# Optimization experiments

Measured on AMD Instinct MI355X. Metric: run time of the kernel, lower is better.

Reference implementation:

```python
import jax, jax.numpy as jnp
import numpy as np

FFT_N = 320.0  # one-sided 161-bin spectrum of a 320-point FFT


def setup_inputs() -> dict:
    key = jax.random.key(0)
    spec = jax.random.normal(key, (32, 4000, 161, 2), dtype=jnp.float32)
    return {"spec": spec}


def _frame_gain(spec):
    # spec: [B, T, F, 2] -> per-frame RMS gain g0: [B, T]
    spec_pow = jnp.sum(spec * spec, axis=-1)  # [B, T, F]
    p = (jnp.sum(spec_pow[..., 1:-1], axis=-1) * 2.0
         + spec_pow[..., 0] + spec_pow[..., -1]) / FFT_N  # [B, T]
    return jnp.sqrt(p)


def _ema_over_time(g0):
    # g[0] = g0[0]; g[n] = 0.9*g[n-1] + 0.1*g0[n]  (scan over time axis 1)
    def step(carry, x):
        c = carry * 0.9 + x * 0.1
        return c, c
    init = g0[:, 0]                       # [B]
    xs = jnp.swapaxes(g0[:, 1:], 0, 1)    # [T-1, B]
    _, outs = jax.lax.scan(step, init, xs)  # [T-1, B]
    return jnp.concatenate([g0[:, :1], jnp.swapaxes(outs, 0, 1)], axis=1)  # [B, T]


def reference(spec):
    g0 = _frame_gain(spec)                        # [B, T]
    gain = _ema_over_time(g0)[:, :, None, None]   # [B, T, 1, 1]
    new_spec = spec / (gain + 0.001)              # [B, T, F, 2]
    return new_spec, gain
```

## Files before the change

### kernel.cpp

```cpp
#include <hip/hip_runtime.h>


typedef float f32x4 __attribute__((ext_vector_type(4)));
typedef float f32x2 __attribute__((ext_vector_type(2)));

#define B_SZ 32
#define T_SZ 4000
#define BINS 161
#define FRAME_F 322
#define FRAMES (B_SZ * T_SZ)
#define N_SPEC ((size_t)FRAMES * FRAME_F)
#define N4 (N_SPEC / 4)
#define EMA_W 384

__global__ __launch_bounds__(256) void k_frame_gain(
    const float* __restrict__ spec, float* __restrict__ g0) {
  int gtid = blockIdx.x * 256 + threadIdx.x;
  int wid  = gtid >> 6;
  int lane = threadIdx.x & 63;
  if (wid >= FRAMES) return;

  const float* fp = spec + (size_t)wid * FRAME_F;

  f32x4 v0 = *(const f32x4*)(fp + lane * 4);
  float s0 = v0.x * v0.x + v0.y * v0.y;
  float s1 = v0.z * v0.z + v0.w * v0.w;
  float acc = 2.0f * (s0 + s1);
  if (lane == 0) acc -= s0;

  if (lane < 16) {
    f32x4 v1 = *(const f32x4*)(fp + (64 + lane) * 4);
    acc += 2.0f * (v1.x * v1.x + v1.y * v1.y + v1.z * v1.z + v1.w * v1.w);
  } else if (lane == 16) {
    f32x2 v2 = *(const f32x2*)(fp + 320);
    acc += v2.x * v2.x + v2.y * v2.y;
  }

#pragma unroll
  for (int off = 32; off > 0; off >>= 1) acc += __shfl_xor(acc, off, 64);
  if (lane == 0) g0[wid] = sqrtf(acc * (1.0f / 320.0f));
}

__global__ __launch_bounds__(256) void k_ema(
    const float* __restrict__ g0, float* __restrict__ gain_out) {
  __shared__ float xs[EMA_W + 256];
  int b  = blockIdx.y;
  int t0 = blockIdx.x * 256;
  int lo = t0 - (EMA_W - 1); if (lo < 0) lo = 0;
  int hi = t0 + 256; if (hi > T_SZ) hi = T_SZ;
  int n  = hi - lo;
  const float* gb = g0 + b * T_SZ;

  for (int i = threadIdx.x; i < n; i += 256) xs[i] = gb[lo + i];
  __syncthreads();

  int t = t0 + (int)threadIdx.x;
  if (t >= T_SZ) return;
  int s = t - (EMA_W - 1); if (s < 1) s = 1;
  float c = (s == 1) ? xs[0] : 0.f;
  for (int k = s; k <= t; ++k) c = c * 0.9f + xs[k - lo] * 0.1f;
  gain_out[b * T_SZ + t] = c;
}

__global__ __launch_bounds__(256) void k_apply(
    const float* __restrict__ spec, const float* __restrict__ gain,
    float* __restrict__ out) {
  size_t i = (size_t)blockIdx.x * 256 + threadIdx.x;
  if (i >= N4) return;
  f32x4 v = ((const f32x4*)spec)[i];
  unsigned p0 = (unsigned)(2 * i);
  unsigned f0 = p0 / 161u;
  unsigned f1 = (p0 + 1) / 161u;
  float inv0 = 1.0f / (gain[f0] + 0.001f);
  float inv1 = 1.0f / (gain[f1] + 0.001f);
  f32x4 r;
  r.x = v.x * inv0; r.y = v.y * inv0;
  r.z = v.z * inv1; r.w = v.w * inv1;
  __builtin_nontemporal_store(r, (f32x4*)out + i);
}

extern "C" void kernel_launch(void* const* d_in, const int* in_sizes, int n_in,
                              void* d_out, int out_size, void* d_ws, size_t ws_size,
                              hipStream_t stream) {
  const float* spec = (const float*)d_in[0];
  float* out  = (float*)d_out;
  float* gain = out + N_SPEC;
  float* g0   = (float*)d_ws;

  int blocks1 = (FRAMES + 3) / 4;
  k_frame_gain<<<blocks1, 256, 0, stream>>>(spec, g0);

  dim3 g2((T_SZ + 255) / 256, B_SZ);
  k_ema<<<g2, 256, 0, stream>>>(g0, gain);

  int blocks3 = (int)((N4 + 255) / 256);
  k_apply<<<blocks3, 256, 0, stream>>>(spec, gain, out);
}
```

Before: 100.2 us.

## Fuse gain, EMA and apply kernels into one cooperative persistent kernel

Replaces the three separate launches (frame gain, EMA, apply) with a single cooperative kernel that uses grid-stride loops and grid.sync() between phases. The aim is to remove the launch gaps between kernels. In exchange, the grid is capped at about 1024 blocks, the grid-wide barriers add cost, and the bandwidth-bound phases run with less occupancy. The grid size assumes 256 CUs.

```diff
diff --git a/kernel.cpp b/kernel.cpp
--- a/kernel.cpp
+++ b/kernel.cpp
@@ -1,4 +1,7 @@
 #include <hip/hip_runtime.h>
+#include <hip/hip_cooperative_groups.h>
+
+namespace cg = cooperative_groups;
 
 
 typedef float f32x4 __attribute__((ext_vector_type(4)));
@@ -6,77 +9,82 @@
 
 #define B_SZ 32
 #define T_SZ 4000
-#define BINS 161
 #define FRAME_F 322
 #define FRAMES (B_SZ * T_SZ)
 #define N_SPEC ((size_t)FRAMES * FRAME_F)
 #define N4 (N_SPEC / 4)
 #define EMA_W 384
+#define BLOCK 256
+#define CHUNKS_PER_B 16
 
-__global__ __launch_bounds__(256) void k_frame_gain(
-    const float* __restrict__ spec, float* __restrict__ g0) {
-  int gtid = blockIdx.x * 256 + threadIdx.x;
-  int wid  = gtid >> 6;
-  int lane = threadIdx.x & 63;
-  if (wid >= FRAMES) return;
+__global__ __launch_bounds__(BLOCK, 4) void k_fused(
+    const float* __restrict__ spec, float* __restrict__ out,
+    float* __restrict__ gain, float* __restrict__ g0) {
+  cg::grid_group grid = cg::this_grid();
+  __shared__ float xs[EMA_W + 256];
 
-  const float* fp = spec + (size_t)wid * FRAME_F;
-
-  f32x4 v0 = *(const f32x4*)(fp + lane * 4);
-  float s0 = v0.x * v0.x + v0.y * v0.y;
-  float s1 = v0.z * v0.z + v0.w * v0.w;
-  float acc = 2.0f * (s0 + s1);
-  if (lane == 0) acc -= s0;
-
-  if (lane < 16) {
-    f32x4 v1 = *(const f32x4*)(fp + (64 + lane) * 4);
-    acc += 2.0f * (v1.x * v1.x + v1.y * v1.y + v1.z * v1.z + v1.w * v1.w);
-  } else if (lane == 16) {
-    f32x2 v2 = *(const f32x2*)(fp + 320);
-    acc += v2.x * v2.x + v2.y * v2.y;
+  {
+    int lane   = threadIdx.x & 63;
+    int wave0  = (blockIdx.x * BLOCK + threadIdx.x) >> 6;
+    int nwaves = (gridDim.x * BLOCK) >> 6;
+    for (int wid = wave0; wid < FRAMES; wid += nwaves) {
+      const float* fp = spec + (size_t)wid * FRAME_F;
+      f32x4 v0 = *(const f32x4*)(fp + lane * 4);
+      float s0 = v0.x * v0.x + v0.y * v0.y;
+      float s1 = v0.z * v0.z + v0.w * v0.w;
+      float acc = 2.0f * (s0 + s1);
+      if (lane == 0) acc -= s0;
+      if (lane < 16) {
+        f32x4 v1 = *(const f32x4*)(fp + (64 + lane) * 4);
+        acc += 2.0f * (v1.x * v1.x + v1.y * v1.y + v1.z * v1.z + v1.w * v1.w);
+      } else if (lane == 16) {
+        f32x2 v2 = *(const f32x2*)(fp + 320);
+        acc += v2.x * v2.x + v2.y * v2.y;
+      }
+#pragma unroll
+      for (int off = 32; off > 0; off >>= 1) acc += __shfl_xor(acc, off, 64);
+      if (lane == 0) g0[wid] = sqrtf(acc * (1.0f / 320.0f));
+    }
   }
 
-#pragma unroll
-  for (int off = 32; off > 0; off >>= 1) acc += __shfl_xor(acc, off, 64);
-  if (lane == 0) g0[wid] = sqrtf(acc * (1.0f / 320.0f));
-}
+  grid.sync();
 
-__global__ __launch_bounds__(256) void k_ema(
-    const float* __restrict__ g0, float* __restrict__ gain_out) {
-  __shared__ float xs[EMA_W + 256];
-  int b  = blockIdx.y;
-  int t0 = blockIdx.x * 256;
-  int lo = t0 - (EMA_W - 1); if (lo < 0) lo = 0;
-  int hi = t0 + 256; if (hi > T_SZ) hi = T_SZ;
-  int n  = hi - lo;
-  const float* gb = g0 + b * T_SZ;
+  for (int u = blockIdx.x; u < B_SZ * CHUNKS_PER_B; u += gridDim.x) {
+    int b  = u >> 4;
+    int t0 = (u & 15) * 256;
+    int lo = t0 - (EMA_W - 1); if (lo < 0) lo = 0;
+    int hi = t0 + 256; if (hi > T_SZ) hi = T_SZ;
+    int n  = hi - lo;
+    const float* gb = g0 + b * T_SZ;
+    __syncthreads();
+    for (int i = threadIdx.x; i < n; i += BLOCK) xs[i] = gb[lo + i];
+    __syncthreads();
+    int t = t0 + (int)threadIdx.x;
+    if (t < T_SZ) {
+      int s = t - (EMA_W - 1); if (s < 1) s = 1;
+      float c = (s == 1) ? xs[0] : 0.f;
+      for (int k = s; k <= t; ++k) c = c * 0.9f + xs[k - lo] * 0.1f;
+      gain[b * T_SZ + t] = c;
+    }
+  }
 
-  for (int i = threadIdx.x; i < n; i += 256) xs[i] = gb[lo + i];
-  __syncthreads();
+  grid.sync();
 
-  int t = t0 + (int)threadIdx.x;
-  if (t >= T_SZ) return;
-  int s = t - (EMA_W - 1); if (s < 1) s = 1;
-  float c = (s == 1) ? xs[0] : 0.f;
-  for (int k = s; k <= t; ++k) c = c * 0.9f + xs[k - lo] * 0.1f;
-  gain_out[b * T_SZ + t] = c;
-}
-
-__global__ __launch_bounds__(256) void k_apply(
-    const float* __restrict__ spec, const float* __restrict__ gain,
-    float* __restrict__ out) {
-  size_t i = (size_t)blockIdx.x * 256 + threadIdx.x;
-  if (i >= N4) return;
-  f32x4 v = ((const f32x4*)spec)[i];
-  unsigned p0 = (unsigned)(2 * i);
-  unsigned f0 = p0 / 161u;
-  unsigned f1 = (p0 + 1) / 161u;
-  float inv0 = 1.0f / (gain[f0] + 0.001f);
-  float inv1 = 1.0f / (gain[f1] + 0.001f);
-  f32x4 r;
-  r.x = v.x * inv0; r.y = v.y * inv0;
-  r.z = v.z * inv1; r.w = v.w * inv1;
-  __builtin_nontemporal_store(r, (f32x4*)out + i);
+  {
+    size_t stride = (size_t)gridDim.x * BLOCK;
+    for (size_t i = (size_t)blockIdx.x * BLOCK + threadIdx.x; i < N4; i += stride) {
+      f32x4 v = ((const f32x4*)spec)[i];
+      unsigned p0 = (unsigned)(2 * i);
+      unsigned f0 = p0 / 161u;
+      unsigned f1 = (p0 + 1) / 161u;
+      float inv0 = 1.0f / (gain[f0] + 0.001f);
+      float inv1 = 1.0f / (gain[f1] + 0.001f);
+      f32x4 r;
+      r.x = v.x * inv0; r.y = v.y * inv0;
+      r.z = v.z * inv1; r.w = v.w * inv1;
+      __builtin_nontemporal_store(r, (f32x4*)out + i);
+    }
+  }
 }
 
 extern "C" void kernel_launch(void* const* d_in, const int* in_sizes, int n_in,
@@ -87,12 +95,13 @@
   float* gain = out + N_SPEC;
   float* g0   = (float*)d_ws;
 
-  int blocks1 = (FRAMES + 3) / 4;
-  k_frame_gain<<<blocks1, 256, 0, stream>>>(spec, g0);
+  int maxb_per_cu = 4;
+  (void)hipOccupancyMaxActiveBlocksPerMultiprocessor(&maxb_per_cu, (const void*)k_fused, BLOCK, 0);
+  if (maxb_per_cu < 1) maxb_per_cu = 1;
+  int grid = maxb_per_cu * 256;
+  if (grid > 1024) grid = 1024;
 
-  dim3 g2((T_SZ + 255) / 256, B_SZ);
-  k_ema<<<g2, 256, 0, stream>>>(g0, gain);
-
-  int blocks3 = (int)((N4 + 255) / 256);
-  k_apply<<<blocks3, 256, 0, stream>>>(spec, gain, out);
+  void* args[] = {(void*)&spec, (void*)&out, (void*)&gain, (void*)&g0};
+  hipLaunchCooperativeKernel((void*)k_fused, dim3(grid), dim3(BLOCK),
+                             args, 0, stream);
 }
```

After: 289.7 us. 189% more time.

## Fuse EMA scan into apply kernel with per-chunk reciprocal gains in LDS

Applied to the files above, without the earlier changes.

Merges the EMA kernel and the scaling kernel into one kernel. Each block handles a 100-frame chunk of one batch, recomputes the truncated EMA for those frames from a halo in shared memory, stores reciprocal gains in LDS, and then scales the chunk's spectrum. This removes one launch, the global gain reads and the per-element divisions, and uses a cheaper frame-index computation. In exchange the grid is only 1280 blocks, and most threads sit idle while 100 of them run the serial EMA loop of up to 384 steps before streaming begins.

```diff
diff --git a/kernel.cpp b/kernel.cpp
--- a/kernel.cpp
+++ b/kernel.cpp
@@ -6,28 +6,29 @@
 
 #define B_SZ 32
 #define T_SZ 4000
-#define BINS 161
 #define FRAME_F 322
 #define FRAMES (B_SZ * T_SZ)
 #define N_SPEC ((size_t)FRAMES * FRAME_F)
-#define N4 (N_SPEC / 4)
 #define EMA_W 384
+#define HALO (EMA_W - 1)
+#define BLOCK 256
+#define CHUNK 100
+#define CHUNKS_PER_B (T_SZ / CHUNK)
+#define C4 (CHUNK * FRAME_F / 4)
 
-__global__ __launch_bounds__(256) void k_frame_gain(
+__global__ __launch_bounds__(BLOCK) void k_frame_gain(
     const float* __restrict__ spec, float* __restrict__ g0) {
-  int gtid = blockIdx.x * 256 + threadIdx.x;
+  int gtid = blockIdx.x * BLOCK + threadIdx.x;
   int wid  = gtid >> 6;
   int lane = threadIdx.x & 63;
   if (wid >= FRAMES) return;
 
   const float* fp = spec + (size_t)wid * FRAME_F;
-
   f32x4 v0 = *(const f32x4*)(fp + lane * 4);
   float s0 = v0.x * v0.x + v0.y * v0.y;
   float s1 = v0.z * v0.z + v0.w * v0.w;
   float acc = 2.0f * (s0 + s1);
   if (lane == 0) acc -= s0;
-
   if (lane < 16) {
     f32x4 v1 = *(const f32x4*)(fp + (64 + lane) * 4);
     acc += 2.0f * (v1.x * v1.x + v1.y * v1.y + v1.z * v1.z + v1.w * v1.w);
@@ -35,48 +36,55 @@
     f32x2 v2 = *(const f32x2*)(fp + 320);
     acc += v2.x * v2.x + v2.y * v2.y;
   }
-
 #pragma unroll
   for (int off = 32; off > 0; off >>= 1) acc += __shfl_xor(acc, off, 64);
   if (lane == 0) g0[wid] = sqrtf(acc * (1.0f / 320.0f));
 }
 
-__global__ __launch_bounds__(256) void k_ema(
-    const float* __restrict__ g0, float* __restrict__ gain_out) {
-  __shared__ float xs[EMA_W + 256];
+__global__ __launch_bounds__(BLOCK) void k_ema_apply(
+    const float* __restrict__ spec, const float* __restrict__ g0,
+    float* __restrict__ out, float* __restrict__ gain_out) {
+  __shared__ float xs[HALO + CHUNK];
+  __shared__ float inv_s[CHUNK];
+
+  int c  = blockIdx.x;
   int b  = blockIdx.y;
-  int t0 = blockIdx.x * 256;
-  int lo = t0 - (EMA_W - 1); if (lo < 0) lo = 0;
-  int hi = t0 + 256; if (hi > T_SZ) hi = T_SZ;
-  int n  = hi - lo;
+  int t0 = c * CHUNK;
+  int lo = t0 - HALO; if (lo < 0) lo = 0;
+  int n  = t0 + CHUNK - lo;
+  int tid = threadIdx.x;
+
   const float* gb = g0 + b * T_SZ;
-
-  for (int i = threadIdx.x; i < n; i += 256) xs[i] = gb[lo + i];
+  for (int i = tid; i < n; i += BLOCK) xs[i] = gb[lo + i];
   __syncthreads();
 
-  int t = t0 + (int)threadIdx.x;
-  if (t >= T_SZ) return;
-  int s = t - (EMA_W - 1); if (s < 1) s = 1;
-  float c = (s == 1) ? xs[0] : 0.f;
-  for (int k = s; k <= t; ++k) c = c * 0.9f + xs[k - lo] * 0.1f;
-  gain_out[b * T_SZ + t] = c;
-}
+  if (tid < CHUNK) {
+    int t = t0 + tid;
+    int s = t - HALO; if (s < 1) s = 1;
+    float cc = (s == 1) ? xs[0] : 0.f;
+    for (int k = s; k <= t; ++k) cc = cc * 0.9f + xs[k - lo] * 0.1f;
+    gain_out[b * T_SZ + t] = cc;
+    inv_s[tid] = 1.0f / (cc + 0.001f);
+  }
+  __syncthreads();
 
-__global__ __launch_bounds__(256) void k_apply(
-    const float* __restrict__ spec, const float* __restrict__ gain,
-    float* __restrict__ out) {
-  size_t i = (size_t)blockIdx.x * 256 + threadIdx.x;
-  if (i >= N4) return;
-  f32x4 v = ((const f32x4*)spec)[i];
-  unsigned p0 = (unsigned)(2 * i);
-  unsigned f0 = p0 / 161u;
-  unsigned f1 = (p0 + 1) / 161u;
-  float inv0 = 1.0f / (gain[f0] + 0.001f);
-  float inv1 = 1.0f / (gain[f1] + 0.001f);
-  f32x4 r;
-  r.x = v.x * inv0; r.y = v.y * inv0;
-  r.z = v.z * inv1; r.w = v.w * inv1;
-  __builtin_nontemporal_store(r, (f32x4*)out + i);
+  size_t base4 = ((size_t)b * T_SZ + t0) * FRAME_F / 4;
+  const f32x4* sp = (const f32x4*)spec + base4;
+  f32x4*       op = (f32x4*)out  + base4;
+#pragma unroll 4
+  for (int i = tid; i < C4; i += BLOCK) {
+    f32x4 v = sp[i];
+    unsigned p0 = (unsigned)(2 * i);
+    unsigned lf = p0 / 161u;
+    unsigned r  = p0 - lf * 161u;
+    unsigned lf1 = lf + (r == 160u);
+    float i0 = inv_s[lf];
+    float i1 = inv_s[lf1];
+    f32x4 rr;
+    rr.x = v.x * i0; rr.y = v.y * i0;
+    rr.z = v.z * i1; rr.w = v.w * i1;
+    __builtin_nontemporal_store(rr, op + i);
+  }
 }
 
 extern "C" void kernel_launch(void* const* d_in, const int* in_sizes, int n_in,
@@ -88,11 +96,8 @@
   float* g0   = (float*)d_ws;
 
   int blocks1 = (FRAMES + 3) / 4;
-  k_frame_gain<<<blocks1, 256, 0, stream>>>(spec, g0);
+  k_frame_gain<<<blocks1, BLOCK, 0, stream>>>(spec, g0);
 
-  dim3 g2((T_SZ + 255) / 256, B_SZ);
-  k_ema<<<g2, 256, 0, stream>>>(g0, gain);
-
-  int blocks3 = (int)((N4 + 255) / 256);
-  k_apply<<<blocks3, 256, 0, stream>>>(spec, gain, out);
+  dim3 g23(CHUNKS_PER_B, B_SZ);
+  k_ema_apply<<<g23, BLOCK, 0, stream>>>(spec, g0, out, gain);
 }
```

New measurement: 101.2 us. No clear change (+1.0%).
